# Kernel optimization log

Measured on AMD Instinct MI355X. Metric: run time of the kernel, lower is better.

The kernel has to match this reference:

```python
import jax, jax.numpy as jnp
import numpy as np

C = 32
H = 8

def _layernorm(x, scale, bias, eps=1e-5):
    mu = jnp.mean(x, axis=-1, keepdims=True)
    var = jnp.mean(jnp.square(x - mu), axis=-1, keepdims=True)
    return (x - mu) * jax.lax.rsqrt(var + eps) * scale + bias


def setup_inputs() -> dict:
    key = jax.random.key(0)
    ks = jax.random.split(key, 10)
    B, s, i, j = 1, 128, 256, 256
    m = jax.random.normal(ks[0], (B, s, i, C), dtype=jnp.float32)
    z = jax.random.normal(ks[1], (B, i, j, C), dtype=jnp.float32)
    sd = 1.0 / np.sqrt(C)
    return {
        "m": m,
        "z": z,
        "ln_scale": jnp.ones((C,), jnp.float32),
        "ln_bias": jnp.zeros((C,), jnp.float32),
        "lnb_scale": jnp.ones((C,), jnp.float32),
        "lnb_bias": jnp.zeros((C,), jnp.float32),
        "wq": jax.random.normal(ks[2], (C, C * H), jnp.float32) * sd,
        "wk": jax.random.normal(ks[3], (C, C * H), jnp.float32) * sd,
        "wv": jax.random.normal(ks[4], (C, C * H), jnp.float32) * sd,
        "wb": jax.random.normal(ks[5], (C, H), jnp.float32) * sd,
        "wg": jax.random.normal(ks[6], (C, C * H), jnp.float32) * sd,
        "wo": jax.random.normal(ks[7], (C * H, C), jnp.float32) * (1.0 / np.sqrt(C * H)),
        "bo": jnp.zeros((C,), jnp.float32),
    }


def reference(m, z, ln_scale, ln_bias, lnb_scale, lnb_bias, wq, wk, wv, wb, wg, wo, bo):
    B, s, i, _ = m.shape
    j = z.shape[2]
    mn = _layernorm(m, ln_scale, ln_bias)                      # (B,s,i,c)
    q = (mn @ wq).reshape(B, s, i, H, C)                        # (B,s,i,h,c)
    k = (mn @ wk).reshape(B, s, i, H, C)
    v = (mn @ wv).reshape(B, s, i, H, C)
    gate = jax.nn.sigmoid(mn @ wg).reshape(B, s, i, H, C)       # (B,s,i,h,c)
    b = (_layernorm(z, lnb_scale, lnb_bias) @ wb)               # (B,i,j,h)
    a = jnp.einsum('bsihc,bsjhc->bsijh', q, k) * (C ** -0.5) + b[:, None]
    a = jax.nn.softmax(a, axis=-2)                              # softmax over j
    o = gate * jnp.einsum('bsijh,bsjhc->bsihc', a, v)
    o = o.reshape(B, s, i, H * C)
    return o @ wo + bo
```

## Files before the change

### kernel.cpp

```cpp
#include <hip/hip_runtime.h>

constexpr int NC = 32;
constexpr int NH = 8;
constexpr int NS = 128;
constexpr int NI = 256;
constexpr int NJ = 256;
constexpr float LN_EPS = 1e-5f;
constexpr float QSCALE = 0.17677669529663687f;
constexpr float LOG2E  = 1.4426950408889634f;

typedef __bf16 bf16x8 __attribute__((ext_vector_type(8)));
typedef __bf16 bf16x2 __attribute__((ext_vector_type(2)));
typedef float floatx4 __attribute__((ext_vector_type(4)));

__device__ __forceinline__ float fexp2(float x) {
#if __has_builtin(__builtin_amdgcn_exp2f)
    return __builtin_amdgcn_exp2f(x);
#else
    return exp2f(x);
#endif
}
__device__ __forceinline__ float frcp(float x) {
#if __has_builtin(__builtin_amdgcn_rcpf)
    return __builtin_amdgcn_rcpf(x);
#else
    return 1.0f / x;
#endif
}
__device__ __forceinline__ unsigned pk2c(float a, float b) {
    union { bf16x2 v; unsigned u; } c;
    c.v = bf16x2{(__bf16)a, (__bf16)b};
    return c.u;
}
__device__ __forceinline__ unsigned pkbb(__bf16 a, __bf16 b) {
    union { bf16x2 v; unsigned u; } c;
    c.v = bf16x2{a, b};
    return c.u;
}

__device__ __forceinline__ int qkOff(int row, int chunk) {
    return row * 32 + ((chunk ^ ((row >> 1) & 3)) << 3);
}
__device__ __forceinline__ int vOff(int c, int chunk) {
    return c * 256 + ((chunk ^ (c & 7)) << 3);
}

__global__ __launch_bounds__(256) void biasprep_kernel(
    const float* __restrict__ z, const float* __restrict__ lnb_s,
    const float* __restrict__ lnb_b, const float* __restrict__ wb,
    const float* __restrict__ wq, const float* __restrict__ wk,
    const float* __restrict__ wv, const float* __restrict__ wg,
    const float* __restrict__ wo,
    float* __restrict__ bias32, unsigned short* __restrict__ wprep,
    unsigned short* __restrict__ wofrag)
{
    const int b = blockIdx.x;
    const int t = threadIdx.x;
    if (b < 256) {
        __shared__ float zL[256 * 33];
        const float4* src = (const float4*)(z + (size_t)b * NJ * NC);
#pragma unroll
        for (int k = 0; k < 8; ++k) {
            int idx = t + 256 * k;
            float4 v = src[idx];
            int f = idx * 4;
            int j = f >> 5, c = f & 31;
            zL[j * 33 + c]     = v.x; zL[j * 33 + c + 1] = v.y;
            zL[j * 33 + c + 2] = v.z; zL[j * 33 + c + 3] = v.w;
        }
        __syncthreads();

        float x[NC];
#pragma unroll
        for (int c = 0; c < NC; ++c) x[c] = zL[t * 33 + c];
        float mu = 0.f;
#pragma unroll
        for (int c = 0; c < NC; ++c) mu += x[c];
        mu *= (1.0f / NC);
        float var = 0.f;
#pragma unroll
        for (int c = 0; c < NC; ++c) { float d = x[c] - mu; var += d * d; }
        var *= (1.0f / NC);
        float rs = rsqrtf(var + LN_EPS);
        float acc[NH];
#pragma unroll
        for (int h = 0; h < NH; ++h) acc[h] = 0.f;
#pragma unroll
        for (int c = 0; c < NC; ++c) {
            float xn = (x[c] - mu) * rs * lnb_s[c] + lnb_b[c];
#pragma unroll
            for (int h = 0; h < NH; ++h) acc[h] += xn * wb[c * NH + h];
        }
        const int i = b;
        const int w_ = i >> 6, it = (i >> 4) & 3, lm = i & 15;
        const int jc = t >> 5, jt = (t >> 4) & 1, lq = (t >> 2) & 3, r = t & 3;
        const int base = jc * 8192 + w_ * 2048 + (jt * 4 + it) * 256
                       + (lq * 16 + lm) * 4 + r;
#pragma unroll
        for (int h = 0; h < NH; ++h)
            bias32[h * 65536 + base] = acc[h] * LOG2E;
    } else if (b < 272) {
        int g = (b - 256) * 256 + t;
        int p  = g >> 10;
        int h  = (g >> 7) & 7;
        int ct = (g >> 6) & 1;
        int l  = g & 63;
        const float* W = (p == 0) ? wq : (p == 1) ? wk : (p == 2) ? wv : wg;
        float scale = (p == 0) ? QSCALE * LOG2E : (p == 3) ? LOG2E : 1.0f;
        int col = 32 * h + 16 * ct + (l & 15);
        int r0  = 8 * (l >> 4);
        float v[8];
#pragma unroll
        for (int e = 0; e < 8; ++e) v[e] = W[(r0 + e) * 256 + col] * scale;
        uint4 u;
        u.x = pk2c(v[0], v[1]); u.y = pk2c(v[2], v[3]);
        u.z = pk2c(v[4], v[5]); u.w = pk2c(v[6], v[7]);
        *(uint4*)&wprep[g * 8] = u;
    } else {
        int g = (b - 272) * 256 + t;
        int tile = g >> 6;
        int l = g & 63;
        int kt = tile >> 1, nt = tile & 1;
        int r0 = kt * 32 + 8 * (l >> 4);
        int col = nt * 16 + (l & 15);
        float v[8];
#pragma unroll
        for (int e = 0; e < 8; ++e) v[e] = wo[(r0 + e) * 32 + col];
        uint4 u;
        u.x = pk2c(v[0], v[1]); u.y = pk2c(v[2], v[3]);
        u.z = pk2c(v[4], v[5]); u.w = pk2c(v[6], v[7]);
        *(uint4*)&wofrag[g * 8] = u;
    }
}

__global__ __launch_bounds__(256, 3) void attn_kernel(
    const float* __restrict__ m, const float* __restrict__ ln_s,
    const float* __restrict__ ln_b,
    const unsigned short* __restrict__ wprep,
    const float* __restrict__ bias32,
    unsigned short* __restrict__ attn16)
{
    __shared__ unsigned short QPX[256 * 32];
    __shared__ unsigned short Kt[256 * 32];
    __shared__ unsigned short Vt[32 * 256];

    const int t = threadIdx.x;
    const int h = blockIdx.x & 7;
    const int s = blockIdx.x >> 3;
    const int l = t & 63, w = t >> 6;
    const int lm = l & 15, lq = l >> 4;
    const int ibase = w * 64;
    const floatx4 zero = {0.f, 0.f, 0.f, 0.f};

    {
        const float4* mr = (const float4*)(m + ((size_t)s * NI + t) * NC);
        float x[NC];
#pragma unroll
        for (int k = 0; k < 8; ++k) {
            float4 v = mr[k];
            x[4*k] = v.x; x[4*k+1] = v.y; x[4*k+2] = v.z; x[4*k+3] = v.w;
        }
        float mu = 0.f;
#pragma unroll
        for (int c = 0; c < NC; ++c) mu += x[c];
        mu *= (1.0f / NC);
        float var = 0.f;
#pragma unroll
        for (int c = 0; c < NC; ++c) { float d = x[c] - mu; var += d * d; }
        var *= (1.0f / NC);
        float rs = rsqrtf(var + LN_EPS);
#pragma unroll
        for (int k = 0; k < 4; ++k) {
            uint4 u;
            u.x = pk2c((x[8*k+0]-mu)*rs*ln_s[8*k+0]+ln_b[8*k+0],
                       (x[8*k+1]-mu)*rs*ln_s[8*k+1]+ln_b[8*k+1]);
            u.y = pk2c((x[8*k+2]-mu)*rs*ln_s[8*k+2]+ln_b[8*k+2],
                       (x[8*k+3]-mu)*rs*ln_s[8*k+3]+ln_b[8*k+3]);
            u.z = pk2c((x[8*k+4]-mu)*rs*ln_s[8*k+4]+ln_b[8*k+4],
                       (x[8*k+5]-mu)*rs*ln_s[8*k+5]+ln_b[8*k+5]);
            u.w = pk2c((x[8*k+6]-mu)*rs*ln_s[8*k+6]+ln_b[8*k+6],
                       (x[8*k+7]-mu)*rs*ln_s[8*k+7]+ln_b[8*k+7]);
            *(uint4*)&QPX[qkOff(t, k)] = u;
        }
    }

    const unsigned short* wp = wprep + ((size_t)h * 128 + l) * 8;
    bf16x8 wfQ[2], wfK[2], wfV[2];
#pragma unroll
    for (int ct = 0; ct < 2; ++ct) {
        wfQ[ct] = *(const bf16x8*)&wp[(0 * 1024 + ct * 64) * 8];
        wfK[ct] = *(const bf16x8*)&wp[(1 * 1024 + ct * 64) * 8];
        wfV[ct] = *(const bf16x8*)&wp[(2 * 1024 + ct * 64) * 8];
    }
    bf16x8 Xb[4];
#pragma unroll
    for (int it = 0; it < 4; ++it)
        Xb[it] = *(const bf16x8*)&QPX[qkOff(ibase + it * 16 + lm, lq)];

#pragma unroll
    for (int it = 0; it < 4; ++it)
#pragma unroll
        for (int ct = 0; ct < 2; ++ct) {
            floatx4 d = __builtin_amdgcn_mfma_f32_16x16x32_bf16(wfQ[ct], Xb[it], zero, 0, 0, 0);
            uint2 u; u.x = pk2c(d[0], d[1]); u.y = pk2c(d[2], d[3]);
            int row = ibase + it * 16 + lm;
            *(uint2*)&QPX[qkOff(row, 2 * ct + (lq >> 1)) + (lq & 1) * 4] = u;
        }
#pragma unroll
    for (int it = 0; it < 4; ++it)
#pragma unroll
        for (int ct = 0; ct < 2; ++ct) {
            floatx4 d = __builtin_amdgcn_mfma_f32_16x16x32_bf16(wfK[ct], Xb[it], zero, 0, 0, 0);
            uint2 u; u.x = pk2c(d[0], d[1]); u.y = pk2c(d[2], d[3]);
            int row = ibase + it * 16 + lm;
            *(uint2*)&Kt[qkOff(row, 2 * ct + (lq >> 1)) + (lq & 1) * 4] = u;
        }
#pragma unroll
    for (int jt = 0; jt < 4; ++jt)
#pragma unroll
        for (int ct = 0; ct < 2; ++ct) {
            floatx4 d = __builtin_amdgcn_mfma_f32_16x16x32_bf16(Xb[jt], wfV[ct], zero, 0, 0, 0);
            uint2 u; u.x = pk2c(d[0], d[1]); u.y = pk2c(d[2], d[3]);
            int c = ct * 16 + lm;
            int chunk = 8 * w + 2 * jt + (lq >> 1);
            *(uint2*)&Vt[vOff(c, chunk) + (lq & 1) * 4] = u;
        }

    bf16x8 Qb[4];
#pragma unroll
    for (int it = 0; it < 4; ++it)
        Qb[it] = *(const bf16x8*)&QPX[qkOff(ibase + it * 16 + lm, lq)];

    __syncthreads();

    floatx4 accO[2][4];
#pragma unroll
    for (int ct = 0; ct < 2; ++ct)
#pragma unroll
        for (int it = 0; it < 4; ++it) accO[ct][it] = zero;
    floatx4 accL[4];
#pragma unroll
    for (int it = 0; it < 4; ++it) accL[it] = zero;
    bf16x8 ones;
#pragma unroll
    for (int e = 0; e < 8; ++e) ones[e] = (__bf16)1.0f;

    const float* bptr = bias32 + (size_t)h * 65536 + w * 2048 + l * 4;

    for (int jc = 0; jc < 8; ++jc) {
        const int j0 = jc * 32;
        const float* bj = bptr + jc * 8192;

#pragma unroll
        for (int jt = 0; jt < 2; ++jt) {
            bf16x8 Ka = *(const bf16x8*)&Kt[qkOff(j0 + jt * 16 + lm, lq)];
#pragma unroll
            for (int it = 0; it < 4; ++it) {
                floatx4 C = *(const floatx4*)(bj + (jt * 4 + it) * 256);
                floatx4 S = __builtin_amdgcn_mfma_f32_16x16x32_bf16(Ka, Qb[it], C, 0, 0, 0);
                __bf16 p0 = (__bf16)fexp2(S[0]);
                __bf16 p1 = (__bf16)fexp2(S[1]);
                __bf16 p2 = (__bf16)fexp2(S[2]);
                __bf16 p3 = (__bf16)fexp2(S[3]);
                uint2 u; u.x = pkbb(p0, p1); u.y = pkbb(p2, p3);
                int row = ibase + it * 16 + lm;
                *(uint2*)&QPX[qkOff(row, 2 * jt + (lq >> 1)) + (lq & 1) * 4] = u;
            }
        }

        bf16x8 Va0 = *(const bf16x8*)&Vt[vOff(lm, 4 * jc + lq)];
        bf16x8 Va1 = *(const bf16x8*)&Vt[vOff(16 + lm, 4 * jc + lq)];
#pragma unroll
        for (int it = 0; it < 4; ++it) {
            bf16x8 Pb = *(const bf16x8*)&QPX[qkOff(ibase + it * 16 + lm, lq)];
            accO[0][it] = __builtin_amdgcn_mfma_f32_16x16x32_bf16(Va0, Pb, accO[0][it], 0, 0, 0);
            accO[1][it] = __builtin_amdgcn_mfma_f32_16x16x32_bf16(Va1, Pb, accO[1][it], 0, 0, 0);
            accL[it]    = __builtin_amdgcn_mfma_f32_16x16x32_bf16(ones, Pb, accL[it], 0, 0, 0);
        }
    }

    float gt[2][4][4];
    {
        bf16x8 wfG0 = *(const bf16x8*)&wp[(3 * 1024 + 0 * 64) * 8];
        bf16x8 wfG1 = *(const bf16x8*)&wp[(3 * 1024 + 1 * 64) * 8];
#pragma unroll
        for (int it = 0; it < 4; ++it) {
            floatx4 d0 = __builtin_amdgcn_mfma_f32_16x16x32_bf16(wfG0, Xb[it], zero, 0, 0, 0);
            floatx4 d1 = __builtin_amdgcn_mfma_f32_16x16x32_bf16(wfG1, Xb[it], zero, 0, 0, 0);
#pragma unroll
            for (int r = 0; r < 4; ++r) {
                gt[0][it][r] = frcp(1.0f + fexp2(-d0[r]));
                gt[1][it][r] = frcp(1.0f + fexp2(-d1[r]));
            }
        }
    }
#pragma unroll
    for (int it = 0; it < 4; ++it) {
        const float inv = frcp(accL[it][0]);
        const size_t rowb = ((size_t)s * NI + ibase + it * 16 + lm) * 256 + h * 32;
#pragma unroll
        for (int ct = 0; ct < 2; ++ct) {
            float o0 = accO[ct][it][0] * inv * gt[ct][it][0];
            float o1 = accO[ct][it][1] * inv * gt[ct][it][1];
            float o2 = accO[ct][it][2] * inv * gt[ct][it][2];
            float o3 = accO[ct][it][3] * inv * gt[ct][it][3];
            uint2 u; u.x = pk2c(o0, o1); u.y = pk2c(o2, o3);
            *(uint2*)&attn16[rowb + ct * 16 + lq * 4] = u;
        }
    }
}

__global__ __launch_bounds__(256) void proj_kernel(
    const unsigned short* __restrict__ attn16,
    const unsigned short* __restrict__ wofrag,
    const float* __restrict__ bo, float* __restrict__ out)
{
    const int t = threadIdx.x;
    const int l = t & 63, w = t >> 6;
    const int lm = l & 15, lq = l >> 4;
    const int row0 = blockIdx.x * 128 + w * 32;
    const floatx4 zero = {0.f, 0.f, 0.f, 0.f};

    floatx4 acc[2][2];
#pragma unroll
    for (int it = 0; it < 2; ++it)
#pragma unroll
        for (int nt = 0; nt < 2; ++nt) acc[it][nt] = zero;

#pragma unroll 2
    for (int kt = 0; kt < 8; ++kt) {
        bf16x8 a0 = *(const bf16x8*)&attn16[(size_t)(row0 + lm) * 256 + kt * 32 + lq * 8];
        bf16x8 a1 = *(const bf16x8*)&attn16[(size_t)(row0 + 16 + lm) * 256 + kt * 32 + lq * 8];
        bf16x8 b0 = *(const bf16x8*)&wofrag[((kt * 2 + 0) * 64 + l) * 8];
        bf16x8 b1 = *(const bf16x8*)&wofrag[((kt * 2 + 1) * 64 + l) * 8];
        acc[0][0] = __builtin_amdgcn_mfma_f32_16x16x32_bf16(a0, b0, acc[0][0], 0, 0, 0);
        acc[0][1] = __builtin_amdgcn_mfma_f32_16x16x32_bf16(a0, b1, acc[0][1], 0, 0, 0);
        acc[1][0] = __builtin_amdgcn_mfma_f32_16x16x32_bf16(a1, b0, acc[1][0], 0, 0, 0);
        acc[1][1] = __builtin_amdgcn_mfma_f32_16x16x32_bf16(a1, b1, acc[1][1], 0, 0, 0);
    }

    float bov[2] = {bo[lm], bo[16 + lm]};
#pragma unroll
    for (int it = 0; it < 2; ++it)
#pragma unroll
        for (int nt = 0; nt < 2; ++nt)
#pragma unroll
            for (int r = 0; r < 4; ++r)
                out[(size_t)(row0 + it * 16 + lq * 4 + r) * NC + nt * 16 + lm]
                    = acc[it][nt][r] + bov[nt];
}

extern "C" void kernel_launch(void* const* d_in, const int* in_sizes, int n_in,
                              void* d_out, int out_size, void* d_ws, size_t ws_size,
                              hipStream_t stream) {
    const float* m     = (const float*)d_in[0];
    const float* z     = (const float*)d_in[1];
    const float* ln_s  = (const float*)d_in[2];
    const float* ln_b  = (const float*)d_in[3];
    const float* lnb_s = (const float*)d_in[4];
    const float* lnb_b = (const float*)d_in[5];
    const float* wq    = (const float*)d_in[6];
    const float* wk    = (const float*)d_in[7];
    const float* wv    = (const float*)d_in[8];
    const float* wb    = (const float*)d_in[9];
    const float* wg    = (const float*)d_in[10];
    const float* wo    = (const float*)d_in[11];
    const float* bo    = (const float*)d_in[12];
    float* out = (float*)d_out;

    float* bias32 = (float*)d_ws;
    unsigned short* wprep  = (unsigned short*)((char*)d_ws + (2u << 20));
    unsigned short* wofrag = (unsigned short*)((char*)d_ws + (2u << 20) + 65536);
    unsigned short* attn16 = (unsigned short*)((char*)d_ws + (2u << 20) + 65536 + 16384);

    biasprep_kernel<<<276, 256, 0, stream>>>(z, lnb_s, lnb_b, wb, wq, wk, wv, wg,
                                             wo, bias32, wprep, wofrag);
    attn_kernel<<<NS * NH, 256, 0, stream>>>(m, ln_s, ln_b, wprep, bias32, attn16);
    proj_kernel<<<(NS * NI) / 128, 256, 0, stream>>>(attn16, wofrag, bo, out);
}
```

Measured before the change: 121.0 us.

## Fuse output projection into attention kernel via per-head atomic accumulation

Removes the separate projection kernel and the bf16 attn16 intermediate buffer. Each attention block stages its gated per-head output in shared memory, multiplies it by that head's slice of wo with MFMA, and atomically adds the partial result into the output. The output is pre-filled with the bias inside the prep kernel. This trades one kernel launch plus about 16MB of global round-trip traffic for 8-way float atomics per output element, a grid-stride bias fill, and non-deterministic summation order.

```diff
diff --git a/kernel.cpp b/kernel.cpp
--- a/kernel.cpp
+++ b/kernel.cpp
@@ -37,6 +37,9 @@
     c.v = bf16x2{a, b};
     return c.u;
 }
+__device__ __forceinline__ void atomAddF32(float* p, float v) {
+    unsafeAtomicAdd(p, v);
+}
 
 __device__ __forceinline__ int qkOff(int row, int chunk) {
     return row * 32 + ((chunk ^ ((row >> 1) & 3)) << 3);
@@ -50,9 +53,9 @@
     const float* __restrict__ lnb_b, const float* __restrict__ wb,
     const float* __restrict__ wq, const float* __restrict__ wk,
     const float* __restrict__ wv, const float* __restrict__ wg,
-    const float* __restrict__ wo,
+    const float* __restrict__ wo, const float* __restrict__ bo,
     float* __restrict__ bias32, unsigned short* __restrict__ wprep,
-    unsigned short* __restrict__ wofrag)
+    unsigned short* __restrict__ wofrag, float* __restrict__ out)
 {
     const int b = blockIdx.x;
     const int t = threadIdx.x;
@@ -131,6 +134,16 @@
         u.z = pk2c(v[4], v[5]); u.w = pk2c(v[6], v[7]);
         *(uint4*)&wofrag[g * 8] = u;
     }
+
+    {
+        const int gtid = b * 256 + t;
+        constexpr int NF4 = NS * NI * NC / 4;
+        for (int idx = gtid; idx < NF4; idx += 276 * 256) {
+            int c4 = (idx & 7) * 4;
+            float4 v = {bo[c4], bo[c4 + 1], bo[c4 + 2], bo[c4 + 3]};
+            ((float4*)out)[idx] = v;
+        }
+    }
 }
 
 __global__ __launch_bounds__(256, 3) void attn_kernel(
@@ -138,7 +151,8 @@
     const float* __restrict__ ln_b,
     const unsigned short* __restrict__ wprep,
     const float* __restrict__ bias32,
-    unsigned short* __restrict__ attn16)
+    const unsigned short* __restrict__ wofrag,
+    float* __restrict__ out)
 {
     __shared__ unsigned short QPX[256 * 32];
     __shared__ unsigned short Kt[256 * 32];
@@ -279,7 +293,6 @@
         }
     }
 
-    float gt[2][4][4];
     {
         bf16x8 wfG0 = *(const bf16x8*)&wp[(3 * 1024 + 0 * 64) * 8];
         bf16x8 wfG1 = *(const bf16x8*)&wp[(3 * 1024 + 1 * 64) * 8];
@@ -287,67 +300,43 @@
         for (int it = 0; it < 4; ++it) {
             floatx4 d0 = __builtin_amdgcn_mfma_f32_16x16x32_bf16(wfG0, Xb[it], zero, 0, 0, 0);
             floatx4 d1 = __builtin_amdgcn_mfma_f32_16x16x32_bf16(wfG1, Xb[it], zero, 0, 0, 0);
+            const float inv = frcp(accL[it][0]);
+            const int row = ibase + it * 16 + lm;
+            {
+                float o0 = accO[0][it][0] * inv * frcp(1.0f + fexp2(-d0[0]));
+                float o1 = accO[0][it][1] * inv * frcp(1.0f + fexp2(-d0[1]));
+                float o2 = accO[0][it][2] * inv * frcp(1.0f + fexp2(-d0[2]));
+                float o3 = accO[0][it][3] * inv * frcp(1.0f + fexp2(-d0[3]));
+                uint2 u; u.x = pk2c(o0, o1); u.y = pk2c(o2, o3);
+                *(uint2*)&QPX[qkOff(row, 0 + (lq >> 1)) + (lq & 1) * 4] = u;
+            }
+            {
+                float o0 = accO[1][it][0] * inv * frcp(1.0f + fexp2(-d1[0]));
+                float o1 = accO[1][it][1] * inv * frcp(1.0f + fexp2(-d1[1]));
+                float o2 = accO[1][it][2] * inv * frcp(1.0f + fexp2(-d1[2]));
+                float o3 = accO[1][it][3] * inv * frcp(1.0f + fexp2(-d1[3]));
+                uint2 u; u.x = pk2c(o0, o1); u.y = pk2c(o2, o3);
+                *(uint2*)&QPX[qkOff(row, 2 + (lq >> 1)) + (lq & 1) * 4] = u;
+            }
+        }
+    }
+
+    {
+        bf16x8 wob0 = *(const bf16x8*)&wofrag[((size_t)(h * 2 + 0) * 64 + l) * 8];
+        bf16x8 wob1 = *(const bf16x8*)&wofrag[((size_t)(h * 2 + 1) * 64 + l) * 8];
+#pragma unroll
+        for (int it = 0; it < 4; ++it) {
+            bf16x8 of = *(const bf16x8*)&QPX[qkOff(ibase + it * 16 + lm, lq)];
+            floatx4 p0 = __builtin_amdgcn_mfma_f32_16x16x32_bf16(of, wob0, zero, 0, 0, 0);
+            floatx4 p1 = __builtin_amdgcn_mfma_f32_16x16x32_bf16(of, wob1, zero, 0, 0, 0);
+            float* orow = out + ((size_t)s * NI + ibase + it * 16 + lq * 4) * NC;
 #pragma unroll
             for (int r = 0; r < 4; ++r) {
-                gt[0][it][r] = frcp(1.0f + fexp2(-d0[r]));
-                gt[1][it][r] = frcp(1.0f + fexp2(-d1[r]));
+                atomAddF32(orow + r * NC + lm,      p0[r]);
+                atomAddF32(orow + r * NC + 16 + lm, p1[r]);
             }
         }
     }
-#pragma unroll
-    for (int it = 0; it < 4; ++it) {
-        const float inv = frcp(accL[it][0]);
-        const size_t rowb = ((size_t)s * NI + ibase + it * 16 + lm) * 256 + h * 32;
-#pragma unroll
-        for (int ct = 0; ct < 2; ++ct) {
-            float o0 = accO[ct][it][0] * inv * gt[ct][it][0];
-            float o1 = accO[ct][it][1] * inv * gt[ct][it][1];
-            float o2 = accO[ct][it][2] * inv * gt[ct][it][2];
-            float o3 = accO[ct][it][3] * inv * gt[ct][it][3];
-            uint2 u; u.x = pk2c(o0, o1); u.y = pk2c(o2, o3);
-            *(uint2*)&attn16[rowb + ct * 16 + lq * 4] = u;
-        }
-    }
-}
-
-__global__ __launch_bounds__(256) void proj_kernel(
-    const unsigned short* __restrict__ attn16,
-    const unsigned short* __restrict__ wofrag,
-    const float* __restrict__ bo, float* __restrict__ out)
-{
-    const int t = threadIdx.x;
-    const int l = t & 63, w = t >> 6;
-    const int lm = l & 15, lq = l >> 4;
-    const int row0 = blockIdx.x * 128 + w * 32;
-    const floatx4 zero = {0.f, 0.f, 0.f, 0.f};
-
-    floatx4 acc[2][2];
-#pragma unroll
-    for (int it = 0; it < 2; ++it)
-#pragma unroll
-        for (int nt = 0; nt < 2; ++nt) acc[it][nt] = zero;
-
-#pragma unroll 2
-    for (int kt = 0; kt < 8; ++kt) {
-        bf16x8 a0 = *(const bf16x8*)&attn16[(size_t)(row0 + lm) * 256 + kt * 32 + lq * 8];
-        bf16x8 a1 = *(const bf16x8*)&attn16[(size_t)(row0 + 16 + lm) * 256 + kt * 32 + lq * 8];
-        bf16x8 b0 = *(const bf16x8*)&wofrag[((kt * 2 + 0) * 64 + l) * 8];
-        bf16x8 b1 = *(const bf16x8*)&wofrag[((kt * 2 + 1) * 64 + l) * 8];
-        acc[0][0] = __builtin_amdgcn_mfma_f32_16x16x32_bf16(a0, b0, acc[0][0], 0, 0, 0);
-        acc[0][1] = __builtin_amdgcn_mfma_f32_16x16x32_bf16(a0, b1, acc[0][1], 0, 0, 0);
-        acc[1][0] = __builtin_amdgcn_mfma_f32_16x16x32_bf16(a1, b0, acc[1][0], 0, 0, 0);
-        acc[1][1] = __builtin_amdgcn_mfma_f32_16x16x32_bf16(a1, b1, acc[1][1], 0, 0, 0);
-    }
-
-    float bov[2] = {bo[lm], bo[16 + lm]};
-#pragma unroll
-    for (int it = 0; it < 2; ++it)
-#pragma unroll
-        for (int nt = 0; nt < 2; ++nt)
-#pragma unroll
-            for (int r = 0; r < 4; ++r)
-                out[(size_t)(row0 + it * 16 + lq * 4 + r) * NC + nt * 16 + lm]
-                    = acc[it][nt][r] + bov[nt];
 }
 
 extern "C" void kernel_launch(void* const* d_in, const int* in_sizes, int n_in,
@@ -371,10 +360,9 @@
     float* bias32 = (float*)d_ws;
     unsigned short* wprep  = (unsigned short*)((char*)d_ws + (2u << 20));
     unsigned short* wofrag = (unsigned short*)((char*)d_ws + (2u << 20) + 65536);
-    unsigned short* attn16 = (unsigned short*)((char*)d_ws + (2u << 20) + 65536 + 16384);
 
     biasprep_kernel<<<276, 256, 0, stream>>>(z, lnb_s, lnb_b, wb, wq, wk, wv, wg,
-                                             wo, bias32, wprep, wofrag);
-    attn_kernel<<<NS * NH, 256, 0, stream>>>(m, ln_s, ln_b, wprep, bias32, attn16);
-    proj_kernel<<<(NS * NI) / 128, 256, 0, stream>>>(attn16, wofrag, bo, out);
-}
+                                             wo, bo, bias32, wprep, wofrag, out);
+    attn_kernel<<<NS * NH, 256, 0, stream>>>(m, ln_s, ln_b, wprep, bias32,
+                                             wofrag, out);
+}
```

Result: slower. 130.3 us (+7.7%).

## Feed softmax probabilities directly from registers into PV MFMA, drop P LDS roundtrip

Applied to the files above, without the earlier changes.

Exponentiated scores now stay in registers: the S accumulator layout is reused as the A operand of 16x16x16 bf16 MFMAs for P·V and the row sums, so P is no longer written to and read back from shared memory. V is stored in a fragment-ordered LDS layout, and Q and K share one buffer, cutting LDS to two arrays. Occupancy is raised to 4 blocks per SM. In exchange it uses twice as many smaller MFMAs for PV, and the output is written as scattered 2-byte stores instead of packed 8-byte stores.

```diff
diff --git a/kernel.cpp b/kernel.cpp
--- a/kernel.cpp
+++ b/kernel.cpp
@@ -12,6 +12,7 @@
 typedef __bf16 bf16x8 __attribute__((ext_vector_type(8)));
 typedef __bf16 bf16x2 __attribute__((ext_vector_type(2)));
 typedef float floatx4 __attribute__((ext_vector_type(4)));
+typedef short short4v __attribute__((ext_vector_type(4)));
 
 __device__ __forceinline__ float fexp2(float x) {
 #if __has_builtin(__builtin_amdgcn_exp2f)
@@ -40,9 +41,6 @@
 
 __device__ __forceinline__ int qkOff(int row, int chunk) {
     return row * 32 + ((chunk ^ ((row >> 1) & 3)) << 3);
-}
-__device__ __forceinline__ int vOff(int c, int chunk) {
-    return c * 256 + ((chunk ^ (c & 7)) << 3);
 }
 
 __global__ __launch_bounds__(256) void biasprep_kernel(
@@ -133,16 +131,15 @@
     }
 }
 
-__global__ __launch_bounds__(256, 3) void attn_kernel(
+__global__ __launch_bounds__(256, 4) void attn_kernel(
     const float* __restrict__ m, const float* __restrict__ ln_s,
     const float* __restrict__ ln_b,
     const unsigned short* __restrict__ wprep,
     const float* __restrict__ bias32,
     unsigned short* __restrict__ attn16)
 {
-    __shared__ unsigned short QPX[256 * 32];
-    __shared__ unsigned short Kt[256 * 32];
-    __shared__ unsigned short Vt[32 * 256];
+    __shared__ unsigned short KX[256 * 32];
+    __shared__ unsigned short VF[32 * 256];
 
     const int t = threadIdx.x;
     const int h = blockIdx.x & 7;
@@ -180,7 +177,7 @@
                        (x[8*k+5]-mu)*rs*ln_s[8*k+5]+ln_b[8*k+5]);
             u.w = pk2c((x[8*k+6]-mu)*rs*ln_s[8*k+6]+ln_b[8*k+6],
                        (x[8*k+7]-mu)*rs*ln_s[8*k+7]+ln_b[8*k+7]);
-            *(uint4*)&QPX[qkOff(t, k)] = u;
+            *(uint4*)&KX[qkOff(t, k)] = u;
         }
     }
 
@@ -195,7 +192,7 @@
     bf16x8 Xb[4];
 #pragma unroll
     for (int it = 0; it < 4; ++it)
-        Xb[it] = *(const bf16x8*)&QPX[qkOff(ibase + it * 16 + lm, lq)];
+        Xb[it] = *(const bf16x8*)&KX[qkOff(ibase + it * 16 + lm, lq)];
 
 #pragma unroll
     for (int it = 0; it < 4; ++it)
@@ -204,8 +201,13 @@
             floatx4 d = __builtin_amdgcn_mfma_f32_16x16x32_bf16(wfQ[ct], Xb[it], zero, 0, 0, 0);
             uint2 u; u.x = pk2c(d[0], d[1]); u.y = pk2c(d[2], d[3]);
             int row = ibase + it * 16 + lm;
-            *(uint2*)&QPX[qkOff(row, 2 * ct + (lq >> 1)) + (lq & 1) * 4] = u;
-        }
+            *(uint2*)&KX[qkOff(row, 2 * ct + (lq >> 1)) + (lq & 1) * 4] = u;
+        }
+    bf16x8 Qb[4];
+#pragma unroll
+    for (int it = 0; it < 4; ++it)
+        Qb[it] = *(const bf16x8*)&KX[qkOff(ibase + it * 16 + lm, lq)];
+
 #pragma unroll
     for (int it = 0; it < 4; ++it)
 #pragma unroll
@@ -213,23 +215,18 @@
             floatx4 d = __builtin_amdgcn_mfma_f32_16x16x32_bf16(wfK[ct], Xb[it], zero, 0, 0, 0);
             uint2 u; u.x = pk2c(d[0], d[1]); u.y = pk2c(d[2], d[3]);
             int row = ibase + it * 16 + lm;
-            *(uint2*)&Kt[qkOff(row, 2 * ct + (lq >> 1)) + (lq & 1) * 4] = u;
-        }
+            *(uint2*)&KX[qkOff(row, 2 * ct + (lq >> 1)) + (lq & 1) * 4] = u;
+        }
+
 #pragma unroll
     for (int jt = 0; jt < 4; ++jt)
 #pragma unroll
         for (int ct = 0; ct < 2; ++ct) {
             floatx4 d = __builtin_amdgcn_mfma_f32_16x16x32_bf16(Xb[jt], wfV[ct], zero, 0, 0, 0);
             uint2 u; u.x = pk2c(d[0], d[1]); u.y = pk2c(d[2], d[3]);
-            int c = ct * 16 + lm;
-            int chunk = 8 * w + 2 * jt + (lq >> 1);
-            *(uint2*)&Vt[vOff(c, chunk) + (lq & 1) * 4] = u;
-        }
-
-    bf16x8 Qb[4];
-#pragma unroll
-    for (int it = 0; it < 4; ++it)
-        Qb[it] = *(const bf16x8*)&QPX[qkOff(ibase + it * 16 + lm, lq)];
+            int tile = (w * 4 + jt) * 2 + ct;
+            *(uint2*)&VF[(tile * 64 + l) * 4] = u;
+        }
 
     __syncthreads();
 
@@ -241,71 +238,51 @@
     floatx4 accL[4];
 #pragma unroll
     for (int it = 0; it < 4; ++it) accL[it] = zero;
-    bf16x8 ones;
-#pragma unroll
-    for (int e = 0; e < 8; ++e) ones[e] = (__bf16)1.0f;
+    short4v onesB;
+#pragma unroll
+    for (int e = 0; e < 4; ++e) onesB[e] = (short)0x3F80;
 
     const float* bptr = bias32 + (size_t)h * 65536 + w * 2048 + l * 4;
 
     for (int jc = 0; jc < 8; ++jc) {
-        const int j0 = jc * 32;
         const float* bj = bptr + jc * 8192;
-
 #pragma unroll
         for (int jt = 0; jt < 2; ++jt) {
-            bf16x8 Ka = *(const bf16x8*)&Kt[qkOff(j0 + jt * 16 + lm, lq)];
+            bf16x8 Ka = *(const bf16x8*)&KX[qkOff(jc * 32 + jt * 16 + lm, lq)];
+            const int J = jc * 2 + jt;
+            short4v Vb0 = *(const short4v*)&VF[((J * 2 + 0) * 64 + l) * 4];
+            short4v Vb1 = *(const short4v*)&VF[((J * 2 + 1) * 64 + l) * 4];
 #pragma unroll
             for (int it = 0; it < 4; ++it) {
                 floatx4 C = *(const floatx4*)(bj + (jt * 4 + it) * 256);
                 floatx4 S = __builtin_amdgcn_mfma_f32_16x16x32_bf16(Ka, Qb[it], C, 0, 0, 0);
-                __bf16 p0 = (__bf16)fexp2(S[0]);
-                __bf16 p1 = (__bf16)fexp2(S[1]);
-                __bf16 p2 = (__bf16)fexp2(S[2]);
-                __bf16 p3 = (__bf16)fexp2(S[3]);
-                uint2 u; u.x = pkbb(p0, p1); u.y = pkbb(p2, p3);
-                int row = ibase + it * 16 + lm;
-                *(uint2*)&QPX[qkOff(row, 2 * jt + (lq >> 1)) + (lq & 1) * 4] = u;
+                union { unsigned u[2]; short4v s4; } pu;
+                pu.u[0] = pkbb((__bf16)fexp2(S[0]), (__bf16)fexp2(S[1]));
+                pu.u[1] = pkbb((__bf16)fexp2(S[2]), (__bf16)fexp2(S[3]));
+                accO[0][it] = __builtin_amdgcn_mfma_f32_16x16x16bf16_1k(pu.s4, Vb0, accO[0][it], 0, 0, 0);
+                accO[1][it] = __builtin_amdgcn_mfma_f32_16x16x16bf16_1k(pu.s4, Vb1, accO[1][it], 0, 0, 0);
+                accL[it]    = __builtin_amdgcn_mfma_f32_16x16x16bf16_1k(pu.s4, onesB, accL[it], 0, 0, 0);
             }
         }
-
-        bf16x8 Va0 = *(const bf16x8*)&Vt[vOff(lm, 4 * jc + lq)];
-        bf16x8 Va1 = *(const bf16x8*)&Vt[vOff(16 + lm, 4 * jc + lq)];
-#pragma unroll
-        for (int it = 0; it < 4; ++it) {
-            bf16x8 Pb = *(const bf16x8*)&QPX[qkOff(ibase + it * 16 + lm, lq)];
-            accO[0][it] = __builtin_amdgcn_mfma_f32_16x16x32_bf16(Va0, Pb, accO[0][it], 0, 0, 0);
-            accO[1][it] = __builtin_amdgcn_mfma_f32_16x16x32_bf16(Va1, Pb, accO[1][it], 0, 0, 0);
-            accL[it]    = __builtin_amdgcn_mfma_f32_16x16x32_bf16(ones, Pb, accL[it], 0, 0, 0);
-        }
-    }
-
-    float gt[2][4][4];
+    }
+
     {
         bf16x8 wfG0 = *(const bf16x8*)&wp[(3 * 1024 + 0 * 64) * 8];
         bf16x8 wfG1 = *(const bf16x8*)&wp[(3 * 1024 + 1 * 64) * 8];
+        __bf16* a16 = (__bf16*)attn16;
 #pragma unroll
         for (int it = 0; it < 4; ++it) {
-            floatx4 d0 = __builtin_amdgcn_mfma_f32_16x16x32_bf16(wfG0, Xb[it], zero, 0, 0, 0);
-            floatx4 d1 = __builtin_amdgcn_mfma_f32_16x16x32_bf16(wfG1, Xb[it], zero, 0, 0, 0);
+            floatx4 g0 = __builtin_amdgcn_mfma_f32_16x16x32_bf16(Xb[it], wfG0, zero, 0, 0, 0);
+            floatx4 g1 = __builtin_amdgcn_mfma_f32_16x16x32_bf16(Xb[it], wfG1, zero, 0, 0, 0);
 #pragma unroll
             for (int r = 0; r < 4; ++r) {
-                gt[0][it][r] = frcp(1.0f + fexp2(-d0[r]));
-                gt[1][it][r] = frcp(1.0f + fexp2(-d1[r]));
+                const float inv = frcp(accL[it][r]);
+                float o0 = accO[0][it][r] * inv * frcp(1.0f + fexp2(-g0[r]));
+                float o1 = accO[1][it][r] * inv * frcp(1.0f + fexp2(-g1[r]));
+                const size_t rowb = ((size_t)s * NI + ibase + it * 16 + lq * 4 + r) * 256 + h * 32;
+                a16[rowb + lm]      = (__bf16)o0;
+                a16[rowb + 16 + lm] = (__bf16)o1;
             }
-        }
-    }
-#pragma unroll
-    for (int it = 0; it < 4; ++it) {
-        const float inv = frcp(accL[it][0]);
-        const size_t rowb = ((size_t)s * NI + ibase + it * 16 + lm) * 256 + h * 32;
-#pragma unroll
-        for (int ct = 0; ct < 2; ++ct) {
-            float o0 = accO[ct][it][0] * inv * gt[ct][it][0];
-            float o1 = accO[ct][it][1] * inv * gt[ct][it][1];
-            float o2 = accO[ct][it][2] * inv * gt[ct][it][2];
-            float o3 = accO[ct][it][3] * inv * gt[ct][it][3];
-            uint2 u; u.x = pk2c(o0, o1); u.y = pk2c(o2, o3);
-            *(uint2*)&attn16[rowb + ct * 16 + lq * 4] = u;
         }
     }
 }
```

Result: slower. 128.3 us (+6.0%).
